# Performance work log

Hardware: AMD Instinct MI355X
Metric: run time of the kernel (lower is better)

Reference implementation:

```python
import jax, jax.numpy as jnp
import numpy as np

DIM = 1024
HEADS = 16
DIM_HEAD = 64
SEQ = 2048
BATCH = 2
SCALE = DIM_HEAD ** -0.5
NEG = -jnp.finfo(jnp.float32).max


def setup_inputs() -> dict:
    key = jax.random.key(0)
    k1, k2, k3 = jax.random.split(key, 3)
    x = jax.random.normal(k1, (BATCH, SEQ, DIM), dtype=jnp.float32)
    w_qkv = jax.random.normal(k2, (DIM, 3 * HEADS * DIM_HEAD), dtype=jnp.float32) * 0.02
    w_out = jax.random.normal(k3, (HEADS * DIM_HEAD, DIM), dtype=jnp.float32) * 0.02
    b_out = jnp.zeros((DIM,), dtype=jnp.float32)
    return {"x": x, "w_qkv": w_qkv, "w_out": w_out, "b_out": b_out}


def reference(x, w_qkv, w_out, b_out):
    b, n, _ = x.shape
    qkv = x @ w_qkv  # [b, n, 3*h*d]
    q, k, v = jnp.split(qkv, 3, axis=-1)
    def to_heads(t):
        return t.reshape(b, n, HEADS, DIM_HEAD).transpose(0, 2, 1, 3)  # b h n d
    q, k, v = to_heads(q), to_heads(k), to_heads(v)
    q = q * SCALE
    dots = jnp.einsum('bhid,bhjd->bhij', q, k)  # materialized [b,h,n,n] scores
    causal_mask = jnp.triu(jnp.ones((n, n), dtype=bool), k=1)
    dots = jnp.where(causal_mask, NEG, dots)
    attn = jax.nn.softmax(dots, axis=-1)
    out = jnp.einsum('bhij,bhjd->bhid', attn, v)
    out = out.transpose(0, 2, 1, 3).reshape(b, n, HEADS * DIM_HEAD)
    return out @ w_out + b_out
```

## Files before the change

kernel.cpp:

```cpp
#include <hip/hip_runtime.h>
#include <cstdint>

typedef __attribute__((ext_vector_type(8))) short bfrag_t;
typedef __attribute__((ext_vector_type(4))) float f32x4_t;

#define MFMA16(a,b,c) __builtin_amdgcn_mfma_f32_16x16x32_bf16((a),(b),(c),0,0,0)

__device__ __forceinline__ unsigned short f2bf(float f){
  unsigned u = __float_as_uint(f);
  unsigned r = u + 0x7fffu + ((u >> 16) & 1u);
  return (unsigned short)(r >> 16);
}

__device__ __forceinline__ unsigned pk2bf(float a, float b){
  unsigned r;
  asm("v_cvt_pk_bf16_f32 %0, %1, %2" : "=v"(r) : "v"(a), "v"(b));
  return r;
}

__device__ __forceinline__ void gload16(const unsigned short* g, unsigned short* l){
  __builtin_amdgcn_global_load_lds(
      (const __attribute__((address_space(1))) unsigned int*)(const void*)g,
      (__attribute__((address_space(3))) unsigned int*)(void*)l,
      16, 0, 0);
}

__global__ __launch_bounds__(256) void k_cvt(const float* __restrict__ in,
                                             unsigned short* __restrict__ out, int n4){
  int i = blockIdx.x*blockDim.x + threadIdx.x;
  int stride = gridDim.x*blockDim.x;
  for(; i < n4; i += stride){
    float4 v = ((const float4*)in)[i];
    ushort4 o;
    o.x = f2bf(v.x); o.y = f2bf(v.y); o.z = f2bf(v.z); o.w = f2bf(v.w);
    ((ushort4*)out)[i] = o;
  }
}

__global__ __launch_bounds__(256) void k_transpose(const float* __restrict__ in,
                                                   unsigned short* __restrict__ out,
                                                   int R, int C){
  __shared__ unsigned short tile[32][33];
  int bc = blockIdx.x*32, br = blockIdx.y*32;
  int tx = threadIdx.x & 31, ty = threadIdx.x >> 5;
  #pragma unroll
  for(int i=0;i<32;i+=8){
    tile[ty+i][tx] = f2bf(in[(size_t)(br+ty+i)*C + bc + tx]);
  }
  __syncthreads();
  #pragma unroll
  for(int i=0;i<32;i+=8){
    out[(size_t)(bc+ty+i)*R + br + tx] = tile[tx][ty+i];
  }
}

template<int SWAP>
__device__ __forceinline__ void gemm128_core(
    const unsigned short* __restrict__ A,
    const unsigned short* __restrict__ Bt,
    int K, int bm, int bn, int tid, int w, int wr, int wc, int col16, int g,
    unsigned short* ldsA, unsigned short* ldsB, f32x4_t (&acc)[4][4])
{
  for(int k0=0; k0<K; k0+=32){
    __syncthreads();
    #pragma unroll
    for(int i=0; i<2; i++){
      int u = i*256 + tid;
      int row = u>>2, s = u&3, gs = s ^ ((row>>1)&3);
      gload16(A + (size_t)(bm+row)*K + k0 + gs*8, ldsA + (i*256 + w*64)*8);
    }
    #pragma unroll
    for(int i=0; i<2; i++){
      int u = i*256 + tid;
      int row = u>>2, s = u&3, gs = s ^ ((row>>1)&3);
      gload16(Bt + (size_t)(bn+row)*K + k0 + gs*8, ldsB + (i*256 + w*64)*8);
    }
    __syncthreads();
    bfrag_t af[4], bfr[4];
    #pragma unroll
    for(int mi=0;mi<4;mi++){
      int row = wr*64 + mi*16 + col16;
      int slot = g ^ ((row>>1)&3);
      af[mi] = *(const bfrag_t*)(ldsA + row*32 + slot*8);
    }
    #pragma unroll
    for(int ni=0;ni<4;ni++){
      int row = wc*64 + ni*16 + col16;
      int slot = g ^ ((row>>1)&3);
      bfr[ni] = *(const bfrag_t*)(ldsB + row*32 + slot*8);
    }
    #pragma unroll
    for(int mi=0;mi<4;mi++)
      #pragma unroll
      for(int ni=0;ni<4;ni++){
        if (SWAP) acc[mi][ni] = MFMA16(bfr[ni], af[mi], acc[mi][ni]);
        else      acc[mi][ni] = MFMA16(af[mi], bfr[ni], acc[mi][ni]);
      }
  }
}

__global__ __launch_bounds__(256) void k_gemm1(
    const unsigned short* __restrict__ A,
    const unsigned short* __restrict__ Bt,
    unsigned short* __restrict__ Qo, unsigned short* __restrict__ Kimg,
    unsigned short* __restrict__ Vimg)
{
  __shared__ unsigned short ldsA[128*32];
  __shared__ unsigned short ldsB[128*32];

  const int tid = threadIdx.x;
  const int lane = tid & 63;
  const int w = tid >> 6;
  const int wr = w >> 1, wc = w & 1;
  const int col16 = lane & 15, g = lane >> 4;
  const int bm = blockIdx.y * 128;
  const int bn = blockIdx.x * 128;
  const int K = 1024;

  f32x4_t acc[4][4];
  #pragma unroll
  for(int i=0;i<4;i++)
    #pragma unroll
    for(int j=0;j<4;j++) acc[i][j] = (f32x4_t)0.0f;

  if (bn < 2048){
    gemm128_core<1>(A, Bt, K, bm, bn, tid, w, wr, wc, col16, g, ldsA, ldsB, acc);
    const int which = bn >> 10;
    #pragma unroll
    for(int mi=0;mi<4;mi++){
      int s_full = bm + wr*64 + mi*16 + col16;
      int b = s_full >> 11, sq = s_full & 2047;
      #pragma unroll
      for(int ni=0;ni<4;ni++){
        int n0 = bn + wc*64 + ni*16 + g*4;
        int h = (n0 & 1023) >> 6;
        int d0 = n0 & 63;
        size_t bh = (size_t)(b*16 + h);
        float v0 = acc[mi][ni][0], v1 = acc[mi][ni][1];
        float v2 = acc[mi][ni][2], v3 = acc[mi][ni][3];
        if (which == 0){
          const float sc = 0.18033688f;
          uint2 pkd; pkd.x = pk2bf(v0*sc, v1*sc); pkd.y = pk2bf(v2*sc, v3*sc);
          *(uint2*)(Qo + (bh*2048 + sq)*64 + d0) = pkd;
        } else {
          int kt = sq >> 6, rr = sq & 63;
          int ks = rr >> 4, c16i = rr & 15;
          int dk = d0 >> 5, g3 = (d0 >> 3) & 3, e0 = d0 & 7;
          uint2 pkd; pkd.x = pk2bf(v0, v1); pkd.y = pk2bf(v2, v3);
          size_t off = bh*131072 + (size_t)kt*4096
                     + (size_t)(ks*2 + dk)*512 + (size_t)(g3*16 + c16i)*8 + e0;
          *(uint2*)(Kimg + off) = pkd;
        }
      }
    }
  } else {
    gemm128_core<0>(A, Bt, K, bm, bn, tid, w, wr, wc, col16, g, ldsA, ldsB, acc);
    #pragma unroll
    for(int mi=0;mi<4;mi++){
      int s0 = bm + wr*64 + mi*16 + g*4;
      int b = s0 >> 11, sq0 = s0 & 2047;
      int kt = sq0 >> 6, sc0 = sq0 & 63;
      int jk = sc0 >> 5, g3 = (sc0 >> 3) & 3, e0 = sc0 & 7;
      #pragma unroll
      for(int ni=0;ni<4;ni++){
        int ncol = bn + wc*64 + ni*16 + col16;
        int h = (ncol & 1023) >> 6;
        int d64 = ncol & 63;
        int nimg = d64 >> 4, c16i = d64 & 15;
        size_t bh = (size_t)(b*16 + h);
        uint2 pkd;
        pkd.x = pk2bf(acc[mi][ni][0], acc[mi][ni][1]);
        pkd.y = pk2bf(acc[mi][ni][2], acc[mi][ni][3]);
        size_t off = bh*131072 + (size_t)kt*4096
                   + (size_t)(nimg*2 + jk)*512 + (size_t)(g3*16 + c16i)*8 + e0;
        *(uint2*)(Vimg + off) = pkd;
      }
    }
  }
}

__global__ __launch_bounds__(256) void k_gemm2(
    const unsigned short* __restrict__ A,
    const unsigned short* __restrict__ Bt,
    float* __restrict__ Co, const float* __restrict__ bias)
{
  __shared__ unsigned short ldsA[64*32];
  __shared__ unsigned short ldsB[128*32];

  const int tid = threadIdx.x;
  const int lane = tid & 63;
  const int w = tid >> 6;
  const int wc = w;
  const int col16 = lane & 15, g = lane >> 4;
  const int bm = blockIdx.y * 64;
  const int bn = blockIdx.x * 128;
  const int K = 1024, N = 1024;

  f32x4_t acc[4][2];
  #pragma unroll
  for(int i=0;i<4;i++)
    #pragma unroll
    for(int j=0;j<2;j++) acc[i][j] = (f32x4_t)0.0f;

  for(int k0=0; k0<K; k0+=32){
    __syncthreads();
    {
      int u = tid;
      int row = u>>2, s = u&3, gs = s ^ ((row>>1)&3);
      gload16(A + (size_t)(bm+row)*K + k0 + gs*8, ldsA + (w*64)*8);
    }
    #pragma unroll
    for(int i=0; i<2; i++){
      int u = i*256 + tid;
      int row = u>>2, s = u&3, gs = s ^ ((row>>1)&3);
      gload16(Bt + (size_t)(bn+row)*K + k0 + gs*8, ldsB + (i*256 + w*64)*8);
    }
    __syncthreads();
    bfrag_t af[4], bfr[2];
    #pragma unroll
    for(int mi=0;mi<4;mi++){
      int row = mi*16 + col16;
      int slot = g ^ ((row>>1)&3);
      af[mi] = *(const bfrag_t*)(ldsA + row*32 + slot*8);
    }
    #pragma unroll
    for(int ni=0;ni<2;ni++){
      int row = wc*32 + ni*16 + col16;
      int slot = g ^ ((row>>1)&3);
      bfr[ni] = *(const bfrag_t*)(ldsB + row*32 + slot*8);
    }
    #pragma unroll
    for(int mi=0;mi<4;mi++)
      #pragma unroll
      for(int ni=0;ni<2;ni++)
        acc[mi][ni] = MFMA16(af[mi], bfr[ni], acc[mi][ni]);
  }

  #pragma unroll
  for(int mi=0;mi<4;mi++){
    int mrow = bm + mi*16 + g*4;
    #pragma unroll
    for(int ni=0;ni<2;ni++){
      int ncol = bn + wc*32 + ni*16 + col16;
      float bb = bias[ncol];
      #pragma unroll
      for(int r=0;r<4;r++){
        Co[(size_t)(mrow+r)*N + ncol] = acc[mi][ni][r] + bb;
      }
    }
  }
}

__global__ __launch_bounds__(256, 4) void k_attn(
    const unsigned short* __restrict__ Q,
    const unsigned short* __restrict__ Kimg,
    const unsigned short* __restrict__ Vimg,
    unsigned short* __restrict__ O)
{
  __shared__ unsigned short kls[2*4096];
  __shared__ unsigned short vls[2*4096];
  __shared__ unsigned short plds[4*1024];
  const int lane = threadIdx.x & 63;
  const int w = threadIdx.x >> 6;
  const int col16 = lane & 15, g = lane >> 4;
  const int bh = blockIdx.x;
  const int y = blockIdx.y;
  const int idx = (y & 7)*4 + (y >> 3);
  const int qt = (idx & 1) ? (31 - (idx >> 1)) : (idx >> 1);
  const int b = bh >> 4, h = bh & 15;

  const unsigned short* Qb = Q    + (size_t)bh*2048*64;
  const unsigned short* Kb = Kimg + (size_t)bh*131072;
  const unsigned short* Vb = Vimg + (size_t)bh*131072;
  char* pw = (char*)(plds + w*1024);

  auto stage = [&](int kt, int bsel){
    const unsigned short* gk = Kb + (size_t)kt*4096;
    const unsigned short* gv = Vb + (size_t)kt*4096;
    unsigned short* lk = kls + bsel*4096;
    unsigned short* lv = vls + bsel*4096;
    #pragma unroll
    for(int c=0;c<2;c++){
      int chunk = w*2 + c;
      int u = chunk*64 + lane;
      gload16(gk + u*8, lk + chunk*512);
      gload16(gv + u*8, lv + chunk*512);
    }
  };

  const int qrow0 = qt*64 + w*16;
  const int nkt = qt + 1;
  const int qi = qrow0 + col16;

  bfrag_t qf[2];
  #pragma unroll
  for(int dk=0;dk<2;dk++)
    qf[dk] = *(const bfrag_t*)(Qb + (size_t)(qrow0 + col16)*64 + dk*32 + g*8);

  f32x4_t oaccT[4];
  #pragma unroll
  for(int n=0;n<4;n++) oaccT[n] = (f32x4_t)0.0f;
  float mrun = -1e30f, lrun = 0.f;

  stage(0, 0);
  __syncthreads();

  #pragma unroll 1
  for(int kt=0; kt<nkt; kt++){
    const int cur = kt & 1;
    if (kt+1 < nkt) stage(kt+1, cur^1);

    const bfrag_t* kb = (const bfrag_t*)(kls + cur*4096);
    const bfrag_t* vb = (const bfrag_t*)(vls + cur*4096);

    f32x4_t sacc[4];
    #pragma unroll
    for(int ks=0; ks<4; ks++){
      bfrag_t kf0 = kb[(ks*2+0)*64 + lane];
      bfrag_t kf1 = kb[(ks*2+1)*64 + lane];
      f32x4_t c = (f32x4_t)0.0f;
      c = MFMA16(kf0, qf[0], c);
      c = MFMA16(kf1, qf[1], c);
      sacc[ks] = c;
    }
    if (kt == qt){
      const int kbase = kt*64;
      #pragma unroll
      for(int ks=0; ks<4; ks++)
        #pragma unroll
        for(int r=0;r<4;r++){
          int kj = kbase + ks*16 + g*4 + r;
          if (kj > qi) sacc[ks][r] = -1e30f;
        }
    }
    float pm = fmaxf(
        fmaxf(fmaxf(fmaxf(sacc[0][0],sacc[0][1]),fmaxf(sacc[0][2],sacc[0][3])),
              fmaxf(fmaxf(sacc[1][0],sacc[1][1]),fmaxf(sacc[1][2],sacc[1][3]))),
        fmaxf(fmaxf(fmaxf(sacc[2][0],sacc[2][1]),fmaxf(sacc[2][2],sacc[2][3])),
              fmaxf(fmaxf(sacc[3][0],sacc[3][1]),fmaxf(sacc[3][2],sacc[3][3]))));
    pm = fmaxf(pm, __shfl_xor(pm, 16));
    pm = fmaxf(pm, __shfl_xor(pm, 32));
    if (!__all(pm - mrun <= 11.5415603f)){
      float mnew = fmaxf(mrun, pm);
      float alpha = __builtin_amdgcn_exp2f(mrun - mnew);
      mrun = mnew;
      lrun *= alpha;
      #pragma unroll
      for(int n=0;n<4;n++)
        #pragma unroll
        for(int r=0;r<4;r++)
          oaccT[n][r] *= alpha;
    }
    float rs = 0.f;
    #pragma unroll
    for(int ks=0; ks<4; ks++){
      float p0 = __builtin_amdgcn_exp2f(sacc[ks][0] - mrun);
      float p1 = __builtin_amdgcn_exp2f(sacc[ks][1] - mrun);
      float p2 = __builtin_amdgcn_exp2f(sacc[ks][2] - mrun);
      float p3 = __builtin_amdgcn_exp2f(sacc[ks][3] - mrun);
      rs += (p0+p1)+(p2+p3);
      unsigned w0 = pk2bf(p0, p1);
      unsigned w1 = pk2bf(p2, p3);
      int byte0 = (col16*128 + (ks*16 + g*4)*2) ^ ((col16&7)<<4);
      unsigned long long wd = ((unsigned long long)w1 << 32) | w0;
      *(unsigned long long*)(pw + byte0) = wd;
    }
    rs += __shfl_xor(rs, 16);
    rs += __shfl_xor(rs, 32);
    lrun += rs;
    bfrag_t pf[2];
    #pragma unroll
    for(int jk=0;jk<2;jk++){
      int byteo = (col16*128 + jk*64 + g*16) ^ ((col16&7)<<4);
      pf[jk] = *(const bfrag_t*)(pw + byteo);
    }
    #pragma unroll
    for(int n=0;n<4;n++){
      bfrag_t v0 = vb[(n*2+0)*64 + lane];
      bfrag_t v1 = vb[(n*2+1)*64 + lane];
      oaccT[n] = MFMA16(v0, pf[0], oaccT[n]);
      oaccT[n] = MFMA16(v1, pf[1], oaccT[n]);
    }
    __syncthreads();
  }

  {
    float inv = 1.0f / lrun;
    size_t obase = ((size_t)(b*2048 + qi))*1024 + (size_t)h*64;
    #pragma unroll
    for(int n=0;n<4;n++){
      uint2 pkd;
      pkd.x = pk2bf(oaccT[n][0]*inv, oaccT[n][1]*inv);
      pkd.y = pk2bf(oaccT[n][2]*inv, oaccT[n][3]*inv);
      *(uint2*)(O + obase + n*16 + g*4) = pkd;
    }
  }
}

extern "C" void kernel_launch(void* const* d_in, const int* in_sizes, int n_in,
                              void* d_out, int out_size, void* d_ws, size_t ws_size,
                              hipStream_t stream){
  const float* x     = (const float*)d_in[0];
  const float* w_qkv = (const float*)d_in[1];
  const float* w_out = (const float*)d_in[2];
  const float* b_out = (const float*)d_in[3];
  float* out = (float*)d_out;

  unsigned char* ws = (unsigned char*)d_ws;
  unsigned short* xbf   = (unsigned short*)(ws);
  unsigned short* wqkvT = (unsigned short*)(ws + (size_t)8*1024*1024);
  unsigned short* woutT = (unsigned short*)(ws + (size_t)14*1024*1024);
  unsigned short* Qb    = (unsigned short*)(ws + (size_t)16*1024*1024);
  unsigned short* Kb    = (unsigned short*)(ws + (size_t)24*1024*1024);
  unsigned short* Vtb   = (unsigned short*)(ws + (size_t)32*1024*1024);
  unsigned short* attno = xbf;

  k_cvt<<<2048, 256, 0, stream>>>(x, xbf, 4096*1024/4);
  k_transpose<<<dim3(3072/32, 1024/32), 256, 0, stream>>>(w_qkv, wqkvT, 1024, 3072);
  k_transpose<<<dim3(1024/32, 1024/32), 256, 0, stream>>>(w_out, woutT, 1024, 1024);
  k_gemm1<<<dim3(24, 32), 256, 0, stream>>>(xbf, wqkvT, Qb, Kb, Vtb);
  k_attn<<<dim3(32, 32), 256, 0, stream>>>(Qb, Kb, Vtb, attno);
  k_gemm2<<<dim3(8, 64), 256, 0, stream>>>(attno, woutT, out, b_out);
}
```

Measured before the change: 130.0 us.

## Process two query tiles per attention block and deepen GEMM k-step to 64

Each attention workgroup now handles two 64-row query tiles (128 rows) and shares every staged K/V tile between both, halving the grid and the K/V LDS traffic per query row. The causal pairing maps blocks to qt2 and 15-qt2 to balance work. Both GEMM kernels now load 64-wide K slices per iteration with an 8-way XOR swizzle, halving the number of barriers. The attention change roughly doubles register use (launch bounds lowered to 2 waves/EU) and the GEMMs use twice the LDS, which may reduce occupancy.

```diff
diff --git a/kernel.cpp b/kernel.cpp
--- a/kernel.cpp
+++ b/kernel.cpp
@@ -54,59 +54,14 @@
   }
 }
 
-template<int SWAP>
-__device__ __forceinline__ void gemm128_core(
-    const unsigned short* __restrict__ A,
-    const unsigned short* __restrict__ Bt,
-    int K, int bm, int bn, int tid, int w, int wr, int wc, int col16, int g,
-    unsigned short* ldsA, unsigned short* ldsB, f32x4_t (&acc)[4][4])
-{
-  for(int k0=0; k0<K; k0+=32){
-    __syncthreads();
-    #pragma unroll
-    for(int i=0; i<2; i++){
-      int u = i*256 + tid;
-      int row = u>>2, s = u&3, gs = s ^ ((row>>1)&3);
-      gload16(A + (size_t)(bm+row)*K + k0 + gs*8, ldsA + (i*256 + w*64)*8);
-    }
-    #pragma unroll
-    for(int i=0; i<2; i++){
-      int u = i*256 + tid;
-      int row = u>>2, s = u&3, gs = s ^ ((row>>1)&3);
-      gload16(Bt + (size_t)(bn+row)*K + k0 + gs*8, ldsB + (i*256 + w*64)*8);
-    }
-    __syncthreads();
-    bfrag_t af[4], bfr[4];
-    #pragma unroll
-    for(int mi=0;mi<4;mi++){
-      int row = wr*64 + mi*16 + col16;
-      int slot = g ^ ((row>>1)&3);
-      af[mi] = *(const bfrag_t*)(ldsA + row*32 + slot*8);
-    }
-    #pragma unroll
-    for(int ni=0;ni<4;ni++){
-      int row = wc*64 + ni*16 + col16;
-      int slot = g ^ ((row>>1)&3);
-      bfr[ni] = *(const bfrag_t*)(ldsB + row*32 + slot*8);
-    }
-    #pragma unroll
-    for(int mi=0;mi<4;mi++)
-      #pragma unroll
-      for(int ni=0;ni<4;ni++){
-        if (SWAP) acc[mi][ni] = MFMA16(bfr[ni], af[mi], acc[mi][ni]);
-        else      acc[mi][ni] = MFMA16(af[mi], bfr[ni], acc[mi][ni]);
-      }
-  }
-}
-
 __global__ __launch_bounds__(256) void k_gemm1(
     const unsigned short* __restrict__ A,
     const unsigned short* __restrict__ Bt,
     unsigned short* __restrict__ Qo, unsigned short* __restrict__ Kimg,
     unsigned short* __restrict__ Vimg)
 {
-  __shared__ unsigned short ldsA[128*32];
-  __shared__ unsigned short ldsB[128*32];
+  __shared__ unsigned short ldsA[128*64];
+  __shared__ unsigned short ldsB[128*64];
 
   const int tid = threadIdx.x;
   const int lane = tid & 63;
@@ -116,6 +71,7 @@
   const int bm = blockIdx.y * 128;
   const int bn = blockIdx.x * 128;
   const int K = 1024;
+  const int SWAP = (bn < 2048) ? 1 : 0;
 
   f32x4_t acc[4][4];
   #pragma unroll
@@ -123,8 +79,53 @@
     #pragma unroll
     for(int j=0;j<4;j++) acc[i][j] = (f32x4_t)0.0f;
 
+  for(int k0=0; k0<K; k0+=64){
+    __syncthreads();
+    #pragma unroll
+    for(int i=0; i<4; i++){
+      int u = i*256 + tid;
+      int row = u>>3, s = u&7, gs = s ^ (row&7);
+      gload16(A + (size_t)(bm+row)*K + k0 + gs*8, ldsA + (i*256 + w*64)*8);
+    }
+    #pragma unroll
+    for(int i=0; i<4; i++){
+      int u = i*256 + tid;
+      int row = u>>3, s = u&7, gs = s ^ (row&7);
+      gload16(Bt + (size_t)(bn+row)*K + k0 + gs*8, ldsB + (i*256 + w*64)*8);
+    }
+    __syncthreads();
+    #pragma unroll
+    for(int kk=0; kk<2; kk++){
+      bfrag_t af[4], bfr[4];
+      #pragma unroll
+      for(int mi=0;mi<4;mi++){
+        int row = wr*64 + mi*16 + col16;
+        int slot = (kk*4 + g) ^ (row&7);
+        af[mi] = *(const bfrag_t*)(ldsA + row*64 + slot*8);
+      }
+      #pragma unroll
+      for(int ni=0;ni<4;ni++){
+        int row = wc*64 + ni*16 + col16;
+        int slot = (kk*4 + g) ^ (row&7);
+        bfr[ni] = *(const bfrag_t*)(ldsB + row*64 + slot*8);
+      }
+      if (SWAP){
+        #pragma unroll
+        for(int mi=0;mi<4;mi++)
+          #pragma unroll
+          for(int ni=0;ni<4;ni++)
+            acc[mi][ni] = MFMA16(bfr[ni], af[mi], acc[mi][ni]);
+      } else {
+        #pragma unroll
+        for(int mi=0;mi<4;mi++)
+          #pragma unroll
+          for(int ni=0;ni<4;ni++)
+            acc[mi][ni] = MFMA16(af[mi], bfr[ni], acc[mi][ni]);
+      }
+    }
+  }
+
   if (bn < 2048){
-    gemm128_core<1>(A, Bt, K, bm, bn, tid, w, wr, wc, col16, g, ldsA, ldsB, acc);
     const int which = bn >> 10;
     #pragma unroll
     for(int mi=0;mi<4;mi++){
@@ -154,7 +155,6 @@
       }
     }
   } else {
-    gemm128_core<0>(A, Bt, K, bm, bn, tid, w, wr, wc, col16, g, ldsA, ldsB, acc);
     #pragma unroll
     for(int mi=0;mi<4;mi++){
       int s0 = bm + wr*64 + mi*16 + g*4;
@@ -184,8 +184,8 @@
     const unsigned short* __restrict__ Bt,
     float* __restrict__ Co, const float* __restrict__ bias)
 {
-  __shared__ unsigned short ldsA[64*32];
-  __shared__ unsigned short ldsB[128*32];
+  __shared__ unsigned short ldsA[64*64];
+  __shared__ unsigned short ldsB[128*64];
 
   const int tid = threadIdx.x;
   const int lane = tid & 63;
@@ -202,38 +202,42 @@
     #pragma unroll
     for(int j=0;j<2;j++) acc[i][j] = (f32x4_t)0.0f;
 
-  for(int k0=0; k0<K; k0+=32){
+  for(int k0=0; k0<K; k0+=64){
     __syncthreads();
-    {
-      int u = tid;
-      int row = u>>2, s = u&3, gs = s ^ ((row>>1)&3);
-      gload16(A + (size_t)(bm+row)*K + k0 + gs*8, ldsA + (w*64)*8);
-    }
     #pragma unroll
     for(int i=0; i<2; i++){
       int u = i*256 + tid;
-      int row = u>>2, s = u&3, gs = s ^ ((row>>1)&3);
+      int row = u>>3, s = u&7, gs = s ^ (row&7);
+      gload16(A + (size_t)(bm+row)*K + k0 + gs*8, ldsA + (i*256 + w*64)*8);
+    }
+    #pragma unroll
+    for(int i=0; i<4; i++){
+      int u = i*256 + tid;
+      int row = u>>3, s = u&7, gs = s ^ (row&7);
       gload16(Bt + (size_t)(bn+row)*K + k0 + gs*8, ldsB + (i*256 + w*64)*8);
     }
     __syncthreads();
-    bfrag_t af[4], bfr[2];
-    #pragma unroll
-    for(int mi=0;mi<4;mi++){
-      int row = mi*16 + col16;
-      int slot = g ^ ((row>>1)&3);
-      af[mi] = *(const bfrag_t*)(ldsA + row*32 + slot*8);
-    }
-    #pragma unroll
-    for(int ni=0;ni<2;ni++){
-      int row = wc*32 + ni*16 + col16;
-      int slot = g ^ ((row>>1)&3);
-      bfr[ni] = *(const bfrag_t*)(ldsB + row*32 + slot*8);
-    }
-    #pragma unroll
-    for(int mi=0;mi<4;mi++)
-      #pragma unroll
-      for(int ni=0;ni<2;ni++)
-        acc[mi][ni] = MFMA16(af[mi], bfr[ni], acc[mi][ni]);
+    #pragma unroll
+    for(int kk=0; kk<2; kk++){
+      bfrag_t af[4], bfr[2];
+      #pragma unroll
+      for(int mi=0;mi<4;mi++){
+        int row = mi*16 + col16;
+        int slot = (kk*4 + g) ^ (row&7);
+        af[mi] = *(const bfrag_t*)(ldsA + row*64 + slot*8);
+      }
+      #pragma unroll
+      for(int ni=0;ni<2;ni++){
+        int row = wc*32 + ni*16 + col16;
+        int slot = (kk*4 + g) ^ (row&7);
+        bfr[ni] = *(const bfrag_t*)(ldsB + row*64 + slot*8);
+      }
+      #pragma unroll
+      for(int mi=0;mi<4;mi++)
+        #pragma unroll
+        for(int ni=0;ni<2;ni++)
+          acc[mi][ni] = MFMA16(af[mi], bfr[ni], acc[mi][ni]);
+    }
   }
 
   #pragma unroll
@@ -251,7 +255,7 @@
   }
 }
 
-__global__ __launch_bounds__(256, 4) void k_attn(
+__global__ __launch_bounds__(256, 2) void k_attn(
     const unsigned short* __restrict__ Q,
     const unsigned short* __restrict__ Kimg,
     const unsigned short* __restrict__ Vimg,
@@ -259,20 +263,20 @@
 {
   __shared__ unsigned short kls[2*4096];
   __shared__ unsigned short vls[2*4096];
-  __shared__ unsigned short plds[4*1024];
+  __shared__ unsigned short plds[8*1024];
   const int lane = threadIdx.x & 63;
   const int w = threadIdx.x >> 6;
   const int col16 = lane & 15, g = lane >> 4;
   const int bh = blockIdx.x;
   const int y = blockIdx.y;
-  const int idx = (y & 7)*4 + (y >> 3);
-  const int qt = (idx & 1) ? (31 - (idx >> 1)) : (idx >> 1);
+  const int qt2 = (y & 8) ? (23 - y) : y;
   const int b = bh >> 4, h = bh & 15;
 
   const unsigned short* Qb = Q    + (size_t)bh*2048*64;
   const unsigned short* Kb = Kimg + (size_t)bh*131072;
   const unsigned short* Vb = Vimg + (size_t)bh*131072;
-  char* pw = (char*)(plds + w*1024);
+  char* pwA = (char*)(plds + w*1024);
+  char* pwB = (char*)(plds + 4096 + w*1024);
 
   auto stage = [&](int kt, int bsel){
     const unsigned short* gk = Kb + (size_t)kt*4096;
@@ -288,51 +292,26 @@
     }
   };
 
-  const int qrow0 = qt*64 + w*16;
-  const int nkt = qt + 1;
-  const int qi = qrow0 + col16;
-
-  bfrag_t qf[2];
-  #pragma unroll
-  for(int dk=0;dk<2;dk++)
-    qf[dk] = *(const bfrag_t*)(Qb + (size_t)(qrow0 + col16)*64 + dk*32 + g*8);
-
-  f32x4_t oaccT[4];
-  #pragma unroll
-  for(int n=0;n<4;n++) oaccT[n] = (f32x4_t)0.0f;
-  float mrun = -1e30f, lrun = 0.f;
-
-  stage(0, 0);
-  __syncthreads();
-
-  #pragma unroll 1
-  for(int kt=0; kt<nkt; kt++){
-    const int cur = kt & 1;
-    if (kt+1 < nkt) stage(kt+1, cur^1);
-
-    const bfrag_t* kb = (const bfrag_t*)(kls + cur*4096);
-    const bfrag_t* vb = (const bfrag_t*)(vls + cur*4096);
-
-    f32x4_t sacc[4];
-    #pragma unroll
-    for(int ks=0; ks<4; ks++){
-      bfrag_t kf0 = kb[(ks*2+0)*64 + lane];
-      bfrag_t kf1 = kb[(ks*2+1)*64 + lane];
-      f32x4_t c = (f32x4_t)0.0f;
-      c = MFMA16(kf0, qf[0], c);
-      c = MFMA16(kf1, qf[1], c);
-      sacc[ks] = c;
-    }
-    if (kt == qt){
-      const int kbase = kt*64;
-      #pragma unroll
-      for(int ks=0; ks<4; ks++)
-        #pragma unroll
-        for(int r=0;r<4;r++){
-          int kj = kbase + ks*16 + g*4 + r;
-          if (kj > qi) sacc[ks][r] = -1e30f;
-        }
-    }
+  const int qrowA = qt2*128 + w*16;
+  const int qrowB = qrowA + 64;
+  const int qiA = qrowA + col16;
+  const int qiB = qrowB + col16;
+  const int nkt = 2*qt2 + 2;
+
+  bfrag_t qfA[2], qfB[2];
+  #pragma unroll
+  for(int dk=0;dk<2;dk++){
+    qfA[dk] = *(const bfrag_t*)(Qb + (size_t)qiA*64 + dk*32 + g*8);
+    qfB[dk] = *(const bfrag_t*)(Qb + (size_t)qiB*64 + dk*32 + g*8);
+  }
+
+  f32x4_t oA[4], oB[4];
+  #pragma unroll
+  for(int n=0;n<4;n++){ oA[n] = (f32x4_t)0.0f; oB[n] = (f32x4_t)0.0f; }
+  float mA = -1e30f, lA = 0.f, mB = -1e30f, lB = 0.f;
+
+  auto softmax_g = [&](f32x4_t (&sacc)[4], float& mrun, float& lrun,
+                       f32x4_t (&oacc)[4], char* pwg, bfrag_t (&pf)[2]){
     float pm = fmaxf(
         fmaxf(fmaxf(fmaxf(sacc[0][0],sacc[0][1]),fmaxf(sacc[0][2],sacc[0][3])),
               fmaxf(fmaxf(sacc[1][0],sacc[1][1]),fmaxf(sacc[1][2],sacc[1][3]))),
@@ -349,7 +328,7 @@
       for(int n=0;n<4;n++)
         #pragma unroll
         for(int r=0;r<4;r++)
-          oaccT[n][r] *= alpha;
+          oacc[n][r] *= alpha;
     }
     float rs = 0.f;
     #pragma unroll
@@ -363,36 +342,96 @@
       unsigned w1 = pk2bf(p2, p3);
       int byte0 = (col16*128 + (ks*16 + g*4)*2) ^ ((col16&7)<<4);
       unsigned long long wd = ((unsigned long long)w1 << 32) | w0;
-      *(unsigned long long*)(pw + byte0) = wd;
+      *(unsigned long long*)(pwg + byte0) = wd;
     }
     rs += __shfl_xor(rs, 16);
     rs += __shfl_xor(rs, 32);
     lrun += rs;
-    bfrag_t pf[2];
     #pragma unroll
     for(int jk=0;jk<2;jk++){
       int byteo = (col16*128 + jk*64 + g*16) ^ ((col16&7)<<4);
-      pf[jk] = *(const bfrag_t*)(pw + byteo);
-    }
+      pf[jk] = *(const bfrag_t*)(pwg + byteo);
+    }
+  };
+
+  stage(0, 0);
+  __syncthreads();
+
+  #pragma unroll 1
+  for(int kt=0; kt<nkt; kt++){
+    const int cur = kt & 1;
+    if (kt+1 < nkt) stage(kt+1, cur^1);
+
+    const bfrag_t* kb = (const bfrag_t*)(kls + cur*4096);
+    const bfrag_t* vb = (const bfrag_t*)(vls + cur*4096);
+    const bool doA = (kt <= 2*qt2);
+
+    f32x4_t saccA[4], saccB[4];
+    #pragma unroll
+    for(int ks=0; ks<4; ks++){
+      bfrag_t kf0 = kb[(ks*2+0)*64 + lane];
+      bfrag_t kf1 = kb[(ks*2+1)*64 + lane];
+      if (doA){
+        f32x4_t c = (f32x4_t)0.0f;
+        c = MFMA16(kf0, qfA[0], c);
+        c = MFMA16(kf1, qfA[1], c);
+        saccA[ks] = c;
+      }
+      f32x4_t d = (f32x4_t)0.0f;
+      d = MFMA16(kf0, qfB[0], d);
+      d = MFMA16(kf1, qfB[1], d);
+      saccB[ks] = d;
+    }
+    const int kbase = kt*64;
+    if (doA && kt == 2*qt2){
+      #pragma unroll
+      for(int ks=0; ks<4; ks++)
+        #pragma unroll
+        for(int r=0;r<4;r++){
+          int kj = kbase + ks*16 + g*4 + r;
+          if (kj > qiA) saccA[ks][r] = -1e30f;
+        }
+    }
+    if (kt == 2*qt2+1){
+      #pragma unroll
+      for(int ks=0; ks<4; ks++)
+        #pragma unroll
+        for(int r=0;r<4;r++){
+          int kj = kbase + ks*16 + g*4 + r;
+          if (kj > qiB) saccB[ks][r] = -1e30f;
+        }
+    }
+    bfrag_t pfA[2], pfB[2];
+    if (doA) softmax_g(saccA, mA, lA, oA, pwA, pfA);
+    softmax_g(saccB, mB, lB, oB, pwB, pfB);
     #pragma unroll
     for(int n=0;n<4;n++){
       bfrag_t v0 = vb[(n*2+0)*64 + lane];
       bfrag_t v1 = vb[(n*2+1)*64 + lane];
-      oaccT[n] = MFMA16(v0, pf[0], oaccT[n]);
-      oaccT[n] = MFMA16(v1, pf[1], oaccT[n]);
+      if (doA){
+        oA[n] = MFMA16(v0, pfA[0], oA[n]);
+        oA[n] = MFMA16(v1, pfA[1], oA[n]);
+      }
+      oB[n] = MFMA16(v0, pfB[0], oB[n]);
+      oB[n] = MFMA16(v1, pfB[1], oB[n]);
     }
     __syncthreads();
   }
 
   {
-    float inv = 1.0f / lrun;
-    size_t obase = ((size_t)(b*2048 + qi))*1024 + (size_t)h*64;
+    float invA = 1.0f / lA;
+    float invB = 1.0f / lB;
+    size_t obA = ((size_t)(b*2048 + qiA))*1024 + (size_t)h*64;
+    size_t obB = ((size_t)(b*2048 + qiB))*1024 + (size_t)h*64;
     #pragma unroll
     for(int n=0;n<4;n++){
-      uint2 pkd;
-      pkd.x = pk2bf(oaccT[n][0]*inv, oaccT[n][1]*inv);
-      pkd.y = pk2bf(oaccT[n][2]*inv, oaccT[n][3]*inv);
-      *(uint2*)(O + obase + n*16 + g*4) = pkd;
+      uint2 pa, pb;
+      pa.x = pk2bf(oA[n][0]*invA, oA[n][1]*invA);
+      pa.y = pk2bf(oA[n][2]*invA, oA[n][3]*invA);
+      pb.x = pk2bf(oB[n][0]*invB, oB[n][1]*invB);
+      pb.y = pk2bf(oB[n][2]*invB, oB[n][3]*invB);
+      *(uint2*)(O + obA + n*16 + g*4) = pa;
+      *(uint2*)(O + obB + n*16 + g*4) = pb;
     }
   }
 }
@@ -419,6 +458,6 @@
   k_transpose<<<dim3(3072/32, 1024/32), 256, 0, stream>>>(w_qkv, wqkvT, 1024, 3072);
   k_transpose<<<dim3(1024/32, 1024/32), 256, 0, stream>>>(w_out, woutT, 1024, 1024);
   k_gemm1<<<dim3(24, 32), 256, 0, stream>>>(xbf, wqkvT, Qb, Kb, Vtb);
-  k_attn<<<dim3(32, 32), 256, 0, stream>>>(Qb, Kb, Vtb, attno);
+  k_attn<<<dim3(32, 16), 256, 0, stream>>>(Qb, Kb, Vtb, attno);
   k_gemm2<<<dim3(8, 64), 256, 0, stream>>>(attno, woutT, out, b_out);
 }
```

Result: slower. 146.4 us (+12.6%).
